# Optimization experiments

Measured on AMD Instinct MI355X. Metric: run time of the kernel, lower is better.

The kernel has to match this reference:

```python
import jax, jax.numpy as jnp
import numpy as np

D_MODEL = 1024
N_EXPERTS = 8
TOP_K = 2
D_FF = 4 * D_MODEL
BATCH, SEQ = 4, 2048


def setup_inputs() -> dict:
    key = jax.random.key(0)
    ks = jax.random.split(key, 7)
    s = 0.02
    return {
        "x": jax.random.normal(ks[0], (BATCH, SEQ, D_MODEL), dtype=jnp.float32),
        "Wg": jax.random.normal(ks[1], (D_MODEL, N_EXPERTS), dtype=jnp.float32) * s,
        "bg": jnp.zeros((N_EXPERTS,), dtype=jnp.float32),
        "W1": jax.random.normal(ks[2], (N_EXPERTS, D_MODEL, D_FF), dtype=jnp.float32) * s,
        "b1": jnp.zeros((N_EXPERTS, D_FF), dtype=jnp.float32),
        "W2": jax.random.normal(ks[3], (N_EXPERTS, D_FF, D_MODEL), dtype=jnp.float32) * s,
        "b2": jnp.zeros((N_EXPERTS, D_MODEL), dtype=jnp.float32),
    }


def reference(x, Wg, bg, W1, b1, W2, b2):
    B, S, D = x.shape
    T = B * S
    xf = x.reshape(T, D)  # [T, d_model]

    # Gating: top-k over softmax probabilities
    gate_logits = xf @ Wg + bg                      # [T, E]
    probs = jax.nn.softmax(gate_logits, axis=-1)
    weights, indices = jax.lax.top_k(probs, TOP_K)  # [T, K] each

    # Dense combine weights c[t, e] = sum_k weights[t,k] * (indices[t,k]==e)
    E = Wg.shape[1]
    c = jnp.zeros((T, E), dtype=x.dtype).at[jnp.arange(T)[:, None], indices].add(weights)

    # All-expert FFN as batched GEMMs (same math as masked per-expert loop)
    h = jnp.einsum('td,edf->etf', xf, W1) + b1[:, None, :]   # [E, T, d_ff]
    a = jax.nn.gelu(h, approximate=False)
    y = jnp.einsum('etf,efd->etd', a, W2) + b2[:, None, :]   # [E, T, d_model]

    out = jnp.einsum('te,etd->td', c, y).reshape(B, S, D)
    return out, gate_logits
```

## Files before the change

kernel.cpp:

```cpp
#include <hip/hip_runtime.h>
#include <hip/hip_bf16.h>
#include <math.h>

#define D_MODEL 1024
#define N_EXP   8
#define D_FF    4096
#define T_TOK   8192
#define NPAIR   (T_TOK * 2)
#define CAP_ROWS (NPAIR + N_EXP * 128)
#define MAX_TILES (CAP_ROWS / 128)

#define CHUNK_STRIDE 1056
#define TILE_BYTES   (8 * CHUNK_STRIDE)

typedef __attribute__((ext_vector_type(4)))  float  f32x4;
typedef __attribute__((ext_vector_type(16))) float  f32x16;
typedef __attribute__((ext_vector_type(8)))  __bf16 bf16x8;
typedef __attribute__((ext_vector_type(4)))  __bf16 bf16x4;

#define OFF_W1T   0
#define OFF_W2T   67108864
#define OFF_H     134217728
#define OFF_XR    276824064
#define OFF_META  312475648
#define M_PAIREXP 0
#define M_PAIRW   65536
#define M_ROW2P   131072
#define M_COUNTS  200704
#define M_PADST   200736
#define M_CURSOR  200768
#define M_T2E     201792
#define M_TROW    202336

__device__ __forceinline__ void async_copy16(const void* g, void* s) {
  __builtin_amdgcn_global_load_lds(
      (const __attribute__((address_space(1))) void*)g,
      (__attribute__((address_space(3))) void*)s, 16, 0, 0);
}

__device__ __forceinline__ float gelu_fast(float v) {
  float u = 1.5957691216057308f * (v + 0.044715f * v * v * v);
  return v * __builtin_amdgcn_rcpf(1.f + __expf(-u));
}

__global__ void k_gate(const float* __restrict__ x, const float* __restrict__ Wg,
                       const float* __restrict__ bg, float* __restrict__ logits_out,
                       int* __restrict__ pairExpert, float* __restrict__ pairW) {
  const int t    = blockIdx.x * 4 + (threadIdx.x >> 6);
  const int lane = threadIdx.x & 63;
  const float* xp = x + (size_t)t * D_MODEL;
  float acc[8];
#pragma unroll
  for (int e = 0; e < 8; e++) acc[e] = 0.f;
#pragma unroll
  for (int i = 0; i < 16; i++) {
    int d = i * 64 + lane;
    float xv = xp[d];
    const float4* wr = (const float4*)(Wg + d * 8);
    float4 w0 = wr[0], w1 = wr[1];
    acc[0] += xv * w0.x; acc[1] += xv * w0.y; acc[2] += xv * w0.z; acc[3] += xv * w0.w;
    acc[4] += xv * w1.x; acc[5] += xv * w1.y; acc[6] += xv * w1.z; acc[7] += xv * w1.w;
  }
#pragma unroll
  for (int e = 0; e < 8; e++)
#pragma unroll
    for (int off = 32; off > 0; off >>= 1) acc[e] += __shfl_down(acc[e], off);
  if (lane == 0) {
    float l[8];
#pragma unroll
    for (int e = 0; e < 8; e++) { l[e] = acc[e] + bg[e]; logits_out[t * 8 + e] = l[e]; }
    float m = l[0];
#pragma unroll
    for (int e = 1; e < 8; e++) m = fmaxf(m, l[e]);
    float p[8], s = 0.f;
#pragma unroll
    for (int e = 0; e < 8; e++) { p[e] = expf(l[e] - m); s += p[e]; }
    float inv = 1.0f / s;
    int i1 = 0;
#pragma unroll
    for (int e = 1; e < 8; e++) if (l[e] > l[i1]) i1 = e;
    int i2 = (i1 == 0) ? 1 : 0;
#pragma unroll
    for (int e = 0; e < 8; e++) if (e != i1 && l[e] > l[i2]) i2 = e;
    pairExpert[t * 2 + 0] = i1; pairW[t * 2 + 0] = p[i1] * inv;
    pairExpert[t * 2 + 1] = i2; pairW[t * 2 + 1] = p[i2] * inv;
  }
}

__global__ void k_init(int* __restrict__ row2pair) {
  int i = blockIdx.x * 256 + threadIdx.x;
  if (i < CAP_ROWS) row2pair[i] = -1;
}

__global__ void k_offsets(const int* __restrict__ pairExpert, int* __restrict__ counts,
                          int* __restrict__ padStart, int* __restrict__ cursor,
                          int* __restrict__ t2e, int* __restrict__ trow) {
  __shared__ int hist[8];
  int tid = threadIdx.x;
  if (tid < 8) hist[tid] = 0;
  __syncthreads();
  for (int i = tid; i < NPAIR; i += 256) atomicAdd(&hist[pairExpert[i]], 1);
  __syncthreads();
  if (tid == 0) {
    int run = 0, nt = 0;
    for (int e = 0; e < 8; e++) {
      counts[e] = hist[e]; padStart[e] = run; cursor[e * 32] = 0;
      int tiles = (hist[e] + 127) >> 7;
      for (int i = 0; i < tiles; i++) { t2e[nt] = e; trow[nt] = run + i * 128; nt++; }
      run += tiles * 128;
    }
    for (; nt < MAX_TILES; nt++) t2e[nt] = -1;
  }
}

__global__ void k_place(const int* __restrict__ pairExpert, const int* __restrict__ padStart,
                        int* __restrict__ cursor, int* __restrict__ row2pair) {
  int p = blockIdx.x * 256 + threadIdx.x;
  if (p >= NPAIR) return;
  int e = pairExpert[p];
  int r = atomicAdd(&cursor[e * 32], 1);
  row2pair[padStart[e] + r] = p;
}

__global__ void k_gather(const float* __restrict__ x, const int* __restrict__ row2pair,
                         __bf16* __restrict__ XR) {
  int row = blockIdx.x;
  int pair = row2pair[row];
  int c = threadIdx.x * 4;
  __bf16* dst = XR + (size_t)row * D_MODEL + c;
  if (pair < 0) {
    bf16x4 z = {(__bf16)0.f, (__bf16)0.f, (__bf16)0.f, (__bf16)0.f};
    *(bf16x4*)dst = z;
  } else {
    int t = pair >> 1;
    float4 v = *(const float4*)(x + (size_t)t * D_MODEL + c);
    bf16x4 o = {(__bf16)v.x, (__bf16)v.y, (__bf16)v.z, (__bf16)v.w};
    *(bf16x4*)dst = o;
  }
}

__global__ void k_convT(const float* __restrict__ in, __bf16* __restrict__ out,
                        int R, int C) {
  __shared__ __bf16 tile[64][68];
  int e = blockIdx.z;
  const float* ip = in + (size_t)e * R * C + (size_t)(blockIdx.y * 64) * C + blockIdx.x * 64;
  __bf16* op = out + (size_t)e * R * C + (size_t)(blockIdx.x * 64) * R + blockIdx.y * 64;
#pragma unroll
  for (int it = 0; it < 4; it++) {
    int idx = it * 1024 + threadIdx.x * 4;
    int lr = idx >> 6, lc = idx & 63;
    float4 v = *(const float4*)(ip + (size_t)lr * C + lc);
    bf16x4 o = {(__bf16)v.x, (__bf16)v.y, (__bf16)v.z, (__bf16)v.w};
    *(bf16x4*)&tile[lr][lc] = o;
  }
  __syncthreads();
#pragma unroll
  for (int it = 0; it < 4; it++) {
    int idx = it * 1024 + threadIdx.x * 4;
    int lc = idx >> 6, lr = idx & 63;
    bf16x4 o = {tile[lr + 0][lc], tile[lr + 1][lc], tile[lr + 2][lc], tile[lr + 3][lc]};
    *(bf16x4*)(op + (size_t)lc * R + lr) = o;
  }
}

__global__ __launch_bounds__(256) void k_gemm1(
    const __bf16* __restrict__ XR, const __bf16* __restrict__ W1T,
    const float* __restrict__ b1, __bf16* __restrict__ H,
    const int* __restrict__ t2e, const int* __restrict__ trow) {
  __shared__ __align__(16) char sA[TILE_BYTES];
  __shared__ __align__(16) char sB[TILE_BYTES];
  const int mt = blockIdx.y;
  const int e = t2e[mt];
  if (e < 0) return;
  const int rowBase = trow[mt];
  const int n0 = blockIdx.x * 128;
  const __bf16* Ab = XR + (size_t)rowBase * D_MODEL;
  const __bf16* Bb = W1T + (size_t)e * D_FF * D_MODEL + (size_t)n0 * D_MODEL;

  const int tid = threadIdx.x;
  const int rA = tid >> 2;
  const int kA = (tid & 3) * 8;
  const int lane = tid & 63;
  const int wave = tid >> 6;
  const int wm = (wave >> 1) * 64, wn = (wave & 1) * 64;
  const int l31 = lane & 31;
  const int half = lane >> 5;

  char* dA0 = sA + wave * CHUNK_STRIDE + lane * 16;
  char* dA1 = sA + (4 + wave) * CHUNK_STRIDE + lane * 16;
  char* dB0 = sB + wave * CHUNK_STRIDE + lane * 16;
  char* dB1 = sB + (4 + wave) * CHUNK_STRIDE + lane * 16;
  int mA0 = wm + l31, mA1 = wm + 32 + l31;
  const char* rA0 = sA + (mA0 >> 4) * CHUNK_STRIDE + (mA0 & 15) * 64 + half * 16;
  const char* rA1 = sA + (mA1 >> 4) * CHUNK_STRIDE + (mA1 & 15) * 64 + half * 16;
  int nB0 = wn + l31, nB1 = wn + 32 + l31;
  const char* rB0 = sB + (nB0 >> 4) * CHUNK_STRIDE + (nB0 & 15) * 64 + half * 16;
  const char* rB1 = sB + (nB1 >> 4) * CHUNK_STRIDE + (nB1 & 15) * 64 + half * 16;

  f32x16 acc[2][2];
#pragma unroll
  for (int i = 0; i < 2; i++)
#pragma unroll
    for (int j = 0; j < 2; j++) acc[i][j] = (f32x16)(0.f);

  for (int k0 = 0; k0 < D_MODEL; k0 += 32) {
    async_copy16(Ab + (size_t)rA * D_MODEL + k0 + kA,        dA0);
    async_copy16(Ab + (size_t)(rA + 64) * D_MODEL + k0 + kA, dA1);
    async_copy16(Bb + (size_t)rA * D_MODEL + k0 + kA,        dB0);
    async_copy16(Bb + (size_t)(rA + 64) * D_MODEL + k0 + kA, dB1);
    __syncthreads();
    bf16x8 af[2][2], bfr[2][2];
#pragma unroll
    for (int kc = 0; kc < 2; kc++) {
      af[0][kc]  = *(const bf16x8*)(rA0 + kc * 32);
      af[1][kc]  = *(const bf16x8*)(rA1 + kc * 32);
      bfr[0][kc] = *(const bf16x8*)(rB0 + kc * 32);
      bfr[1][kc] = *(const bf16x8*)(rB1 + kc * 32);
    }
#pragma unroll
    for (int kc = 0; kc < 2; kc++)
#pragma unroll
      for (int ti = 0; ti < 2; ti++)
#pragma unroll
        for (int tj = 0; tj < 2; tj++)
          acc[ti][tj] = __builtin_amdgcn_mfma_f32_32x32x16_bf16(af[ti][kc], bfr[tj][kc], acc[ti][tj], 0, 0, 0);
    __syncthreads();
  }
  int   colv[2]; float biasv[2];
#pragma unroll
  for (int tj = 0; tj < 2; tj++) {
    colv[tj] = n0 + wn + tj * 32 + l31;
    biasv[tj] = b1[e * D_FF + colv[tj]];
  }
#pragma unroll
  for (int ti = 0; ti < 2; ti++)
#pragma unroll
    for (int r = 0; r < 16; r++) {
      size_t row = (size_t)rowBase + wm + ti * 32 + (r & 3) + 8 * (r >> 2) + 4 * half;
#pragma unroll
      for (int tj = 0; tj < 2; tj++)
        H[row * D_FF + colv[tj]] = (__bf16)gelu_fast(acc[ti][tj][r] + biasv[tj]);
    }
}

__global__ __launch_bounds__(256) void k_gemm2(
    const __bf16* __restrict__ H, const __bf16* __restrict__ W2T,
    const float* __restrict__ b2, float* __restrict__ Ypair,
    const int* __restrict__ row2pair, const float* __restrict__ pairW,
    const int* __restrict__ t2e, const int* __restrict__ trow) {
  __shared__ __align__(16) char sA[TILE_BYTES];
  __shared__ __align__(16) char sB[TILE_BYTES];
  const int b = blockIdx.x;
  const int mt = (b >> 6) * 8 + (b & 7);
  const int nb = (b >> 3) & 7;
  const int e = t2e[mt];
  if (e < 0) return;
  const int rowBase = trow[mt];
  const int n0 = nb * 128;
  const __bf16* Ab = H + (size_t)rowBase * D_FF;
  const __bf16* Bb = W2T + (size_t)e * D_MODEL * D_FF + (size_t)n0 * D_FF;

  const int tid = threadIdx.x;
  const int rA = tid >> 2;
  const int kA = (tid & 3) * 8;
  const int lane = tid & 63;
  const int wave = tid >> 6;
  const int wm = (wave >> 1) * 64, wn = (wave & 1) * 64;
  const int l31 = lane & 31;
  const int half = lane >> 5;

  char* dA0 = sA + wave * CHUNK_STRIDE + lane * 16;
  char* dA1 = sA + (4 + wave) * CHUNK_STRIDE + lane * 16;
  char* dB0 = sB + wave * CHUNK_STRIDE + lane * 16;
  char* dB1 = sB + (4 + wave) * CHUNK_STRIDE + lane * 16;
  int mA0 = wm + l31, mA1 = wm + 32 + l31;
  const char* rA0 = sA + (mA0 >> 4) * CHUNK_STRIDE + (mA0 & 15) * 64 + half * 16;
  const char* rA1 = sA + (mA1 >> 4) * CHUNK_STRIDE + (mA1 & 15) * 64 + half * 16;
  int nB0 = wn + l31, nB1 = wn + 32 + l31;
  const char* rB0 = sB + (nB0 >> 4) * CHUNK_STRIDE + (nB0 & 15) * 64 + half * 16;
  const char* rB1 = sB + (nB1 >> 4) * CHUNK_STRIDE + (nB1 & 15) * 64 + half * 16;

  f32x16 acc[2][2];
#pragma unroll
  for (int i = 0; i < 2; i++)
#pragma unroll
    for (int j = 0; j < 2; j++) acc[i][j] = (f32x16)(0.f);

  for (int k0 = 0; k0 < D_FF; k0 += 32) {
    async_copy16(Ab + (size_t)rA * D_FF + k0 + kA,        dA0);
    async_copy16(Ab + (size_t)(rA + 64) * D_FF + k0 + kA, dA1);
    async_copy16(Bb + (size_t)rA * D_FF + k0 + kA,        dB0);
    async_copy16(Bb + (size_t)(rA + 64) * D_FF + k0 + kA, dB1);
    __syncthreads();
    bf16x8 af[2][2], bfr[2][2];
#pragma unroll
    for (int kc = 0; kc < 2; kc++) {
      af[0][kc]  = *(const bf16x8*)(rA0 + kc * 32);
      af[1][kc]  = *(const bf16x8*)(rA1 + kc * 32);
      bfr[0][kc] = *(const bf16x8*)(rB0 + kc * 32);
      bfr[1][kc] = *(const bf16x8*)(rB1 + kc * 32);
    }
#pragma unroll
    for (int kc = 0; kc < 2; kc++)
#pragma unroll
      for (int ti = 0; ti < 2; ti++)
#pragma unroll
        for (int tj = 0; tj < 2; tj++)
          acc[ti][tj] = __builtin_amdgcn_mfma_f32_32x32x16_bf16(af[ti][kc], bfr[tj][kc], acc[ti][tj], 0, 0, 0);
    __syncthreads();
  }
  int colv[2]; float biasv[2];
#pragma unroll
  for (int tj = 0; tj < 2; tj++) {
    colv[tj] = n0 + wn + tj * 32 + l31;
    biasv[tj] = b2[e * D_MODEL + colv[tj]];
  }
#pragma unroll
  for (int ti = 0; ti < 2; ti++)
#pragma unroll
    for (int r = 0; r < 16; r++) {
      int row = rowBase + wm + ti * 32 + (r & 3) + 8 * (r >> 2) + 4 * half;
      int pair = row2pair[row];
      if (pair < 0) continue;
      float w = pairW[pair];
#pragma unroll
      for (int tj = 0; tj < 2; tj++)
        Ypair[(size_t)pair * D_MODEL + colv[tj]] = w * (acc[ti][tj][r] + biasv[tj]);
    }
}

__global__ void k_combine(const float* __restrict__ Ypair, float* __restrict__ out) {
  size_t idx = (size_t)blockIdx.x * 256 + threadIdx.x;
  size_t t = idx >> 8, c4 = idx & 255;
  const float4* y4 = (const float4*)Ypair;
  float4 a = y4[(2 * t) * 256 + c4];
  float4 b = y4[(2 * t + 1) * 256 + c4];
  float4 o = {a.x + b.x, a.y + b.y, a.z + b.z, a.w + b.w};
  ((float4*)out)[idx] = o;
}

extern "C" void kernel_launch(void* const* d_in, const int* in_sizes, int n_in,
                              void* d_out, int out_size, void* d_ws, size_t ws_size,
                              hipStream_t stream) {
  const float* x  = (const float*)d_in[0];
  const float* Wg = (const float*)d_in[1];
  const float* bg = (const float*)d_in[2];
  const float* W1 = (const float*)d_in[3];
  const float* b1 = (const float*)d_in[4];
  const float* W2 = (const float*)d_in[5];
  const float* b2 = (const float*)d_in[6];
  float* out        = (float*)d_out;
  float* logits_out = out + (size_t)T_TOK * D_MODEL;

  char* ws = (char*)d_ws;
  __bf16* W1T = (__bf16*)(ws + OFF_W1T);
  __bf16* W2T = (__bf16*)(ws + OFF_W2T);
  __bf16* H   = (__bf16*)(ws + OFF_H);
  __bf16* XR  = (__bf16*)(ws + OFF_XR);
  float* Ypair = (float*)(ws + OFF_W1T);
  char* meta = ws + OFF_META;
  int*   pairExpert = (int*)(meta + M_PAIREXP);
  float* pairW      = (float*)(meta + M_PAIRW);
  int*   row2pair   = (int*)(meta + M_ROW2P);
  int*   counts     = (int*)(meta + M_COUNTS);
  int*   padStart   = (int*)(meta + M_PADST);
  int*   cursor     = (int*)(meta + M_CURSOR);
  int*   t2e        = (int*)(meta + M_T2E);
  int*   trow       = (int*)(meta + M_TROW);

  k_convT<<<dim3(D_FF / 64, D_MODEL / 64, N_EXP), 256, 0, stream>>>(W1, W1T, D_MODEL, D_FF);
  k_convT<<<dim3(D_MODEL / 64, D_FF / 64, N_EXP), 256, 0, stream>>>(W2, W2T, D_FF, D_MODEL);

  k_init<<<(CAP_ROWS + 255) / 256, 256, 0, stream>>>(row2pair);
  k_gate<<<T_TOK / 4, 256, 0, stream>>>(x, Wg, bg, logits_out, pairExpert, pairW);
  k_offsets<<<1, 256, 0, stream>>>(pairExpert, counts, padStart, cursor, t2e, trow);
  k_place<<<NPAIR / 256, 256, 0, stream>>>(pairExpert, padStart, cursor, row2pair);
  k_gather<<<CAP_ROWS, 256, 0, stream>>>(x, row2pair, XR);

  k_gemm1<<<dim3(D_FF / 128, MAX_TILES), 256, 0, stream>>>(XR, W1T, b1, H, t2e, trow);
  k_gemm2<<<MAX_TILES * (D_MODEL / 128), 256, 0, stream>>>(H, W2T, b2, Ypair, row2pair, pairW, t2e, trow);
  k_combine<<<(size_t)T_TOK * D_MODEL / 4 / 256, 256, 0, stream>>>(Ypair, out);
}
```

Before: 845.5 us.

## Rewrite expert GEMMs with larger tiles, double-buffered LDS and atomic combine

Both expert GEMMs move to 512-thread blocks with 256-row M tiles, a BK of 128, and XOR-swizzled LDS. Loads are double-buffered asynchronous copies interleaved between MFMA phases and gated by waitcnt and barriers, with raised wave priority around the MFMA sections. This is meant to improve data reuse and hide global-load latency. The second GEMM now atomically adds weighted results into a zeroed output, which removes the Ypair buffer and the combine kernel. The cost is atomic contention, a memset, and non-deterministic float summation order.

After: 952.5 us. 1.13x slower.

```diff
diff --git a/kernel.cpp b/kernel.cpp
--- a/kernel.cpp
+++ b/kernel.cpp
@@ -8,10 +8,8 @@
 #define T_TOK   8192
 #define NPAIR   (T_TOK * 2)
 #define CAP_ROWS (NPAIR + N_EXP * 128)
-#define MAX_TILES (CAP_ROWS / 128)
-
-#define CHUNK_STRIDE 1056
-#define TILE_BYTES   (8 * CHUNK_STRIDE)
+#define MAX_T256 72
+#define BKB 128
 
 typedef __attribute__((ext_vector_type(4)))  float  f32x4;
 typedef __attribute__((ext_vector_type(16))) float  f32x16;
@@ -31,11 +29,18 @@
 #define M_CURSOR  200768
 #define M_T2E     201792
 #define M_TROW    202336
+#define M_TLIM    202880
 
 __device__ __forceinline__ void async_copy16(const void* g, void* s) {
   __builtin_amdgcn_global_load_lds(
       (const __attribute__((address_space(1))) void*)g,
       (__attribute__((address_space(3))) void*)s, 16, 0, 0);
+}
+
+__device__ __forceinline__ void wg_barrier() {
+  asm volatile("" ::: "memory");
+  __builtin_amdgcn_s_barrier();
+  asm volatile("" ::: "memory");
 }
 
 __device__ __forceinline__ float gelu_fast(float v) {
@@ -94,7 +99,8 @@
 
 __global__ void k_offsets(const int* __restrict__ pairExpert, int* __restrict__ counts,
                           int* __restrict__ padStart, int* __restrict__ cursor,
-                          int* __restrict__ t2e, int* __restrict__ trow) {
+                          int* __restrict__ t2e, int* __restrict__ trow,
+                          int* __restrict__ tlim) {
   __shared__ int hist[8];
   int tid = threadIdx.x;
   if (tid < 8) hist[tid] = 0;
@@ -105,11 +111,16 @@
     int run = 0, nt = 0;
     for (int e = 0; e < 8; e++) {
       counts[e] = hist[e]; padStart[e] = run; cursor[e * 32] = 0;
-      int tiles = (hist[e] + 127) >> 7;
-      for (int i = 0; i < tiles; i++) { t2e[nt] = e; trow[nt] = run + i * 128; nt++; }
-      run += tiles * 128;
-    }
-    for (; nt < MAX_TILES; nt++) t2e[nt] = -1;
+      int rows = ((hist[e] + 127) >> 7) << 7;
+      for (int r0 = 0; r0 < rows; r0 += 256) {
+        t2e[nt] = e; trow[nt] = run + r0;
+        int rem = rows - r0;
+        tlim[nt] = rem < 256 ? rem : 256;
+        nt++;
+      }
+      run += rows;
+    }
+    for (; nt < MAX_T256; nt++) t2e[nt] = -1;
   }
 }
 
@@ -163,122 +174,204 @@
   }
 }
 
-__global__ __launch_bounds__(256) void k_gemm1(
+
+__global__ __launch_bounds__(512, 2) void k_gemm1(
     const __bf16* __restrict__ XR, const __bf16* __restrict__ W1T,
     const float* __restrict__ b1, __bf16* __restrict__ H,
-    const int* __restrict__ t2e, const int* __restrict__ trow) {
-  __shared__ __align__(16) char sA[TILE_BYTES];
-  __shared__ __align__(16) char sB[TILE_BYTES];
+    const int* __restrict__ t2e, const int* __restrict__ trow,
+    const int* __restrict__ tlim) {
+  __shared__ __align__(16) char lds[2][65536];
   const int mt = blockIdx.y;
   const int e = t2e[mt];
   if (e < 0) return;
   const int rowBase = trow[mt];
-  const int n0 = blockIdx.x * 128;
-  const __bf16* Ab = XR + (size_t)rowBase * D_MODEL;
-  const __bf16* Bb = W1T + (size_t)e * D_FF * D_MODEL + (size_t)n0 * D_MODEL;
+  const int lim = tlim[mt];
+  const int n0 = blockIdx.x * 256;
 
   const int tid = threadIdx.x;
-  const int rA = tid >> 2;
-  const int kA = (tid & 3) * 8;
-  const int lane = tid & 63;
-  const int wave = tid >> 6;
-  const int wm = (wave >> 1) * 64, wn = (wave & 1) * 64;
-  const int l31 = lane & 31;
-  const int half = lane >> 5;
-
-  char* dA0 = sA + wave * CHUNK_STRIDE + lane * 16;
-  char* dA1 = sA + (4 + wave) * CHUNK_STRIDE + lane * 16;
-  char* dB0 = sB + wave * CHUNK_STRIDE + lane * 16;
-  char* dB1 = sB + (4 + wave) * CHUNK_STRIDE + lane * 16;
-  int mA0 = wm + l31, mA1 = wm + 32 + l31;
-  const char* rA0 = sA + (mA0 >> 4) * CHUNK_STRIDE + (mA0 & 15) * 64 + half * 16;
-  const char* rA1 = sA + (mA1 >> 4) * CHUNK_STRIDE + (mA1 & 15) * 64 + half * 16;
-  int nB0 = wn + l31, nB1 = wn + 32 + l31;
-  const char* rB0 = sB + (nB0 >> 4) * CHUNK_STRIDE + (nB0 & 15) * 64 + half * 16;
-  const char* rB1 = sB + (nB1 >> 4) * CHUNK_STRIDE + (nB1 & 15) * 64 + half * 16;
-
-  f32x16 acc[2][2];
-#pragma unroll
-  for (int i = 0; i < 2; i++)
+  const int l = tid & 63;
+  const int w = tid >> 6;
+  const int wm = (w >> 2) * 128;
+  const int wn = (w & 3) * 64;
+  const int l31 = l & 31;
+  const int rsub = l >> 3;
+  const int sg = (l & 7) ^ rsub;
+
+  const char* srcA[4]; const char* srcB[4];
+#pragma unroll
+  for (int i = 0; i < 4; i++) {
+    int ra = rowBase + 8 * (w + 8 * i) + rsub;
+    if (ra > CAP_ROWS - 1) ra = CAP_ROWS - 1;
+    srcA[i] = (const char*)(XR + (size_t)ra * D_MODEL) + sg * 16;
+    int rb = n0 + 8 * (w + 8 * i) + rsub;
+    srcB[i] = (const char*)(W1T + (size_t)e * ((size_t)D_FF * D_MODEL)
+                                + (size_t)rb * D_MODEL) + sg * 16;
+  }
+  const int axr = ((l >> 5) ^ (l & 7)) << 4;
+
+  f32x16 acc[4][2];
+#pragma unroll
+  for (int i = 0; i < 4; i++)
 #pragma unroll
     for (int j = 0; j < 2; j++) acc[i][j] = (f32x16)(0.f);
 
-  for (int k0 = 0; k0 < D_MODEL; k0 += 32) {
-    async_copy16(Ab + (size_t)rA * D_MODEL + k0 + kA,        dA0);
-    async_copy16(Ab + (size_t)(rA + 64) * D_MODEL + k0 + kA, dA1);
-    async_copy16(Bb + (size_t)rA * D_MODEL + k0 + kA,        dB0);
-    async_copy16(Bb + (size_t)(rA + 64) * D_MODEL + k0 + kA, dB1);
-    __syncthreads();
-    bf16x8 af[2][2], bfr[2][2];
-#pragma unroll
-    for (int kc = 0; kc < 2; kc++) {
-      af[0][kc]  = *(const bf16x8*)(rA0 + kc * 32);
-      af[1][kc]  = *(const bf16x8*)(rA1 + kc * 32);
-      bfr[0][kc] = *(const bf16x8*)(rB0 + kc * 32);
-      bfr[1][kc] = *(const bf16x8*)(rB1 + kc * 32);
-    }
-#pragma unroll
-    for (int kc = 0; kc < 2; kc++)
-#pragma unroll
-      for (int ti = 0; ti < 2; ti++)
-#pragma unroll
-        for (int tj = 0; tj < 2; tj++)
-          acc[ti][tj] = __builtin_amdgcn_mfma_f32_32x32x16_bf16(af[ti][kc], bfr[tj][kc], acc[ti][tj], 0, 0, 0);
-    __syncthreads();
-  }
-  int   colv[2]; float biasv[2];
+  {
+    char* sAw = &lds[0][0];
+    char* sBw = sAw + 32768;
+#pragma unroll
+    for (int i = 0; i < 4; i++) {
+      async_copy16(srcA[i], sAw + (w + 8 * i) * 1024);
+      async_copy16(srcB[i], sBw + (w + 8 * i) * 1024);
+    }
+    asm volatile("s_waitcnt vmcnt(0)" ::: "memory");
+    wg_barrier();
+  }
+
+  bf16x8 A[2][4], B[2][4];
+#pragma unroll 2
+  for (int t = 0; t < 16; t++) {
+    const int slot = t & 1;
+    const char* sAr = &lds[0][0] + slot * 65536;
+    const char* sBr = sAr + 32768;
+    char* sAw = &lds[0][0] + (slot ^ 1) * 65536;
+    char* sBw = sAw + 32768;
+    const bool hn = (t + 1) < 16;
+    const size_t ko = (size_t)(t + 1) * BKB;
+
+    if (hn) {
+      async_copy16(srcA[0] + ko, sAw + w * 1024);
+      async_copy16(srcB[0] + ko, sBw + w * 1024);
+      asm volatile("s_waitcnt vmcnt(2)" ::: "memory");
+    } else {
+      asm volatile("s_waitcnt vmcnt(0)" ::: "memory");
+    }
+    wg_barrier();
+#pragma unroll
+    for (int f = 0; f < 2; f++)
+#pragma unroll
+      for (int kc = 0; kc < 4; kc++)
+        A[f][kc] = *(const bf16x8*)(sAr + (wm + f * 32 + l31) * BKB + (axr ^ (kc << 5)));
+#pragma unroll
+    for (int kc = 0; kc < 4; kc++)
+      B[0][kc] = *(const bf16x8*)(sBr + (wn + l31) * BKB + (axr ^ (kc << 5)));
+    __builtin_amdgcn_s_setprio(1);
+#pragma unroll
+    for (int kc = 0; kc < 4; kc++)
+#pragma unroll
+      for (int f = 0; f < 2; f++)
+        acc[f][0] = __builtin_amdgcn_mfma_f32_32x32x16_bf16(A[f][kc], B[0][kc], acc[f][0], 0, 0, 0);
+    __builtin_amdgcn_s_setprio(0);
+    wg_barrier();
+
+#pragma unroll
+    for (int kc = 0; kc < 4; kc++)
+      B[1][kc] = *(const bf16x8*)(sBr + (wn + 32 + l31) * BKB + (axr ^ (kc << 5)));
+    if (hn) {
+      async_copy16(srcA[1] + ko, sAw + (8 + w) * 1024);
+      async_copy16(srcB[1] + ko, sBw + (8 + w) * 1024);
+    }
+    wg_barrier();
+    __builtin_amdgcn_s_setprio(1);
+#pragma unroll
+    for (int kc = 0; kc < 4; kc++)
+#pragma unroll
+      for (int f = 0; f < 2; f++)
+        acc[f][1] = __builtin_amdgcn_mfma_f32_32x32x16_bf16(A[f][kc], B[1][kc], acc[f][1], 0, 0, 0);
+    __builtin_amdgcn_s_setprio(0);
+    wg_barrier();
+
+#pragma unroll
+    for (int f = 0; f < 2; f++)
+#pragma unroll
+      for (int kc = 0; kc < 4; kc++)
+        A[f][kc] = *(const bf16x8*)(sAr + (wm + 64 + f * 32 + l31) * BKB + (axr ^ (kc << 5)));
+    if (hn) {
+      async_copy16(srcA[2] + ko, sAw + (16 + w) * 1024);
+      async_copy16(srcB[2] + ko, sBw + (16 + w) * 1024);
+    }
+    wg_barrier();
+    __builtin_amdgcn_s_setprio(1);
+#pragma unroll
+    for (int kc = 0; kc < 4; kc++)
+#pragma unroll
+      for (int f = 0; f < 2; f++)
+        acc[2 + f][0] = __builtin_amdgcn_mfma_f32_32x32x16_bf16(A[f][kc], B[0][kc], acc[2 + f][0], 0, 0, 0);
+    __builtin_amdgcn_s_setprio(0);
+    wg_barrier();
+
+    if (hn) {
+      async_copy16(srcA[3] + ko, sAw + (24 + w) * 1024);
+      async_copy16(srcB[3] + ko, sBw + (24 + w) * 1024);
+    }
+    wg_barrier();
+    __builtin_amdgcn_s_setprio(1);
+#pragma unroll
+    for (int kc = 0; kc < 4; kc++)
+#pragma unroll
+      for (int f = 0; f < 2; f++)
+        acc[2 + f][1] = __builtin_amdgcn_mfma_f32_32x32x16_bf16(A[f][kc], B[1][kc], acc[2 + f][1], 0, 0, 0);
+    __builtin_amdgcn_s_setprio(0);
+    wg_barrier();
+  }
+
+  const int half = l >> 5;
+  int colv[2]; float biasv[2];
 #pragma unroll
   for (int tj = 0; tj < 2; tj++) {
     colv[tj] = n0 + wn + tj * 32 + l31;
     biasv[tj] = b1[e * D_FF + colv[tj]];
   }
 #pragma unroll
-  for (int ti = 0; ti < 2; ti++)
+  for (int ti = 0; ti < 4; ti++)
 #pragma unroll
     for (int r = 0; r < 16; r++) {
-      size_t row = (size_t)rowBase + wm + ti * 32 + (r & 3) + 8 * (r >> 2) + 4 * half;
-#pragma unroll
-      for (int tj = 0; tj < 2; tj++)
-        H[row * D_FF + colv[tj]] = (__bf16)gelu_fast(acc[ti][tj][r] + biasv[tj]);
-    }
-}
-
-__global__ __launch_bounds__(256) void k_gemm2(
+      int lr = wm + ti * 32 + (r & 3) + 8 * (r >> 2) + 4 * half;
+      if (lr < lim) {
+        size_t row = (size_t)(rowBase + lr);
+#pragma unroll
+        for (int tj = 0; tj < 2; tj++)
+          H[row * D_FF + colv[tj]] = (__bf16)gelu_fast(acc[ti][tj][r] + biasv[tj]);
+      }
+    }
+}
+
+__global__ __launch_bounds__(512, 2) void k_gemm2(
     const __bf16* __restrict__ H, const __bf16* __restrict__ W2T,
-    const float* __restrict__ b2, float* __restrict__ Ypair,
+    const float* __restrict__ b2, float* __restrict__ out,
     const int* __restrict__ row2pair, const float* __restrict__ pairW,
-    const int* __restrict__ t2e, const int* __restrict__ trow) {
-  __shared__ __align__(16) char sA[TILE_BYTES];
-  __shared__ __align__(16) char sB[TILE_BYTES];
-  const int b = blockIdx.x;
-  const int mt = (b >> 6) * 8 + (b & 7);
-  const int nb = (b >> 3) & 7;
+    const int* __restrict__ t2e, const int* __restrict__ trow,
+    const int* __restrict__ tlim) {
+  __shared__ __align__(16) char lds[2][49152];
+  const int mt = blockIdx.y;
   const int e = t2e[mt];
   if (e < 0) return;
   const int rowBase = trow[mt];
-  const int n0 = nb * 128;
-  const __bf16* Ab = H + (size_t)rowBase * D_FF;
-  const __bf16* Bb = W2T + (size_t)e * D_MODEL * D_FF + (size_t)n0 * D_FF;
+  const int lim = tlim[mt];
+  const int n0 = blockIdx.x * 128;
 
   const int tid = threadIdx.x;
-  const int rA = tid >> 2;
-  const int kA = (tid & 3) * 8;
-  const int lane = tid & 63;
-  const int wave = tid >> 6;
-  const int wm = (wave >> 1) * 64, wn = (wave & 1) * 64;
-  const int l31 = lane & 31;
-  const int half = lane >> 5;
-
-  char* dA0 = sA + wave * CHUNK_STRIDE + lane * 16;
-  char* dA1 = sA + (4 + wave) * CHUNK_STRIDE + lane * 16;
-  char* dB0 = sB + wave * CHUNK_STRIDE + lane * 16;
-  char* dB1 = sB + (4 + wave) * CHUNK_STRIDE + lane * 16;
-  int mA0 = wm + l31, mA1 = wm + 32 + l31;
-  const char* rA0 = sA + (mA0 >> 4) * CHUNK_STRIDE + (mA0 & 15) * 64 + half * 16;
-  const char* rA1 = sA + (mA1 >> 4) * CHUNK_STRIDE + (mA1 & 15) * 64 + half * 16;
-  int nB0 = wn + l31, nB1 = wn + 32 + l31;
-  const char* rB0 = sB + (nB0 >> 4) * CHUNK_STRIDE + (nB0 & 15) * 64 + half * 16;
-  const char* rB1 = sB + (nB1 >> 4) * CHUNK_STRIDE + (nB1 & 15) * 64 + half * 16;
+  const int l = tid & 63;
+  const int w = tid >> 6;
+  const int wm = (w >> 1) * 64;
+  const int wn = (w & 1) * 64;
+  const int l31 = l & 31;
+  const int rsub = l >> 3;
+  const int sg = (l & 7) ^ rsub;
+
+  const char* srcA[4]; const char* srcB[2];
+#pragma unroll
+  for (int i = 0; i < 4; i++) {
+    int ra = rowBase + 8 * (w + 8 * i) + rsub;
+    if (ra > CAP_ROWS - 1) ra = CAP_ROWS - 1;
+    srcA[i] = (const char*)(H + (size_t)ra * D_FF) + sg * 16;
+  }
+#pragma unroll
+  for (int i = 0; i < 2; i++) {
+    int rb = n0 + 8 * (w + 8 * i) + rsub;
+    srcB[i] = (const char*)(W2T + (size_t)e * ((size_t)D_MODEL * D_FF)
+                                + (size_t)rb * D_FF) + sg * 16;
+  }
+  const int axr = ((l >> 5) ^ (l & 7)) << 4;
 
   f32x16 acc[2][2];
 #pragma unroll
@@ -286,29 +379,74 @@
 #pragma unroll
     for (int j = 0; j < 2; j++) acc[i][j] = (f32x16)(0.f);
 
-  for (int k0 = 0; k0 < D_FF; k0 += 32) {
-    async_copy16(Ab + (size_t)rA * D_FF + k0 + kA,        dA0);
-    async_copy16(Ab + (size_t)(rA + 64) * D_FF + k0 + kA, dA1);
-    async_copy16(Bb + (size_t)rA * D_FF + k0 + kA,        dB0);
-    async_copy16(Bb + (size_t)(rA + 64) * D_FF + k0 + kA, dB1);
-    __syncthreads();
-    bf16x8 af[2][2], bfr[2][2];
-#pragma unroll
-    for (int kc = 0; kc < 2; kc++) {
-      af[0][kc]  = *(const bf16x8*)(rA0 + kc * 32);
-      af[1][kc]  = *(const bf16x8*)(rA1 + kc * 32);
-      bfr[0][kc] = *(const bf16x8*)(rB0 + kc * 32);
-      bfr[1][kc] = *(const bf16x8*)(rB1 + kc * 32);
-    }
-#pragma unroll
-    for (int kc = 0; kc < 2; kc++)
-#pragma unroll
-      for (int ti = 0; ti < 2; ti++)
-#pragma unroll
-        for (int tj = 0; tj < 2; tj++)
-          acc[ti][tj] = __builtin_amdgcn_mfma_f32_32x32x16_bf16(af[ti][kc], bfr[tj][kc], acc[ti][tj], 0, 0, 0);
-    __syncthreads();
-  }
+  {
+    char* sAw = &lds[0][0];
+    char* sBw = sAw + 32768;
+#pragma unroll
+    for (int i = 0; i < 4; i++) async_copy16(srcA[i], sAw + (w + 8 * i) * 1024);
+#pragma unroll
+    for (int i = 0; i < 2; i++) async_copy16(srcB[i], sBw + (w + 8 * i) * 1024);
+    asm volatile("s_waitcnt vmcnt(0)" ::: "memory");
+    wg_barrier();
+  }
+
+  bf16x8 A[4], B[2][4];
+#pragma unroll 2
+  for (int t = 0; t < 64; t++) {
+    const int slot = t & 1;
+    const char* sAr = &lds[0][0] + slot * 49152;
+    const char* sBr = sAr + 32768;
+    char* sAw = &lds[0][0] + (slot ^ 1) * 49152;
+    char* sBw = sAw + 32768;
+    const bool hn = (t + 1) < 64;
+    const size_t ko = (size_t)(t + 1) * BKB;
+
+    if (hn) {
+      async_copy16(srcA[0] + ko, sAw + w * 1024);
+      async_copy16(srcB[0] + ko, sBw + w * 1024);
+      async_copy16(srcA[1] + ko, sAw + (8 + w) * 1024);
+      async_copy16(srcB[1] + ko, sBw + (8 + w) * 1024);
+      asm volatile("s_waitcnt vmcnt(4)" ::: "memory");
+    } else {
+      asm volatile("s_waitcnt vmcnt(0)" ::: "memory");
+    }
+    wg_barrier();
+#pragma unroll
+    for (int kc = 0; kc < 4; kc++)
+      A[kc] = *(const bf16x8*)(sAr + (wm + l31) * BKB + (axr ^ (kc << 5)));
+#pragma unroll
+    for (int tj = 0; tj < 2; tj++)
+#pragma unroll
+      for (int kc = 0; kc < 4; kc++)
+        B[tj][kc] = *(const bf16x8*)(sBr + (wn + tj * 32 + l31) * BKB + (axr ^ (kc << 5)));
+    __builtin_amdgcn_s_setprio(1);
+#pragma unroll
+    for (int kc = 0; kc < 4; kc++)
+#pragma unroll
+      for (int tj = 0; tj < 2; tj++)
+        acc[0][tj] = __builtin_amdgcn_mfma_f32_32x32x16_bf16(A[kc], B[tj][kc], acc[0][tj], 0, 0, 0);
+    __builtin_amdgcn_s_setprio(0);
+    wg_barrier();
+
+#pragma unroll
+    for (int kc = 0; kc < 4; kc++)
+      A[kc] = *(const bf16x8*)(sAr + (wm + 32 + l31) * BKB + (axr ^ (kc << 5)));
+    if (hn) {
+      async_copy16(srcA[2] + ko, sAw + (16 + w) * 1024);
+      async_copy16(srcA[3] + ko, sAw + (24 + w) * 1024);
+    }
+    wg_barrier();
+    __builtin_amdgcn_s_setprio(1);
+#pragma unroll
+    for (int kc = 0; kc < 4; kc++)
+#pragma unroll
+      for (int tj = 0; tj < 2; tj++)
+        acc[1][tj] = __builtin_amdgcn_mfma_f32_32x32x16_bf16(A[kc], B[tj][kc], acc[1][tj], 0, 0, 0);
+    __builtin_amdgcn_s_setprio(0);
+    wg_barrier();
+  }
+
+  const int half = l >> 5;
   int colv[2]; float biasv[2];
 #pragma unroll
   for (int tj = 0; tj < 2; tj++) {
@@ -319,24 +457,16 @@
   for (int ti = 0; ti < 2; ti++)
 #pragma unroll
     for (int r = 0; r < 16; r++) {
-      int row = rowBase + wm + ti * 32 + (r & 3) + 8 * (r >> 2) + 4 * half;
-      int pair = row2pair[row];
+      int lr = wm + ti * 32 + (r & 3) + 8 * (r >> 2) + 4 * half;
+      if (lr >= lim) continue;
+      int pair = row2pair[rowBase + lr];
       if (pair < 0) continue;
-      float w = pairW[pair];
+      float pw = pairW[pair];
+      size_t tok = (size_t)(pair >> 1);
 #pragma unroll
       for (int tj = 0; tj < 2; tj++)
-        Ypair[(size_t)pair * D_MODEL + colv[tj]] = w * (acc[ti][tj][r] + biasv[tj]);
-    }
-}
-
-__global__ void k_combine(const float* __restrict__ Ypair, float* __restrict__ out) {
-  size_t idx = (size_t)blockIdx.x * 256 + threadIdx.x;
-  size_t t = idx >> 8, c4 = idx & 255;
-  const float4* y4 = (const float4*)Ypair;
-  float4 a = y4[(2 * t) * 256 + c4];
-  float4 b = y4[(2 * t + 1) * 256 + c4];
-  float4 o = {a.x + b.x, a.y + b.y, a.z + b.z, a.w + b.w};
-  ((float4*)out)[idx] = o;
+        atomicAdd(out + tok * D_MODEL + colv[tj], pw * (acc[ti][tj][r] + biasv[tj]));
+    }
 }
 
 extern "C" void kernel_launch(void* const* d_in, const int* in_sizes, int n_in,
@@ -357,7 +487,6 @@
   __bf16* W2T = (__bf16*)(ws + OFF_W2T);
   __bf16* H   = (__bf16*)(ws + OFF_H);
   __bf16* XR  = (__bf16*)(ws + OFF_XR);
-  float* Ypair = (float*)(ws + OFF_W1T);
   char* meta = ws + OFF_META;
   int*   pairExpert = (int*)(meta + M_PAIREXP);
   float* pairW      = (float*)(meta + M_PAIRW);
@@ -367,17 +496,20 @@
   int*   cursor     = (int*)(meta + M_CURSOR);
   int*   t2e        = (int*)(meta + M_T2E);
   int*   trow       = (int*)(meta + M_TROW);
+  int*   tlim       = (int*)(meta + M_TLIM);
+
+  hipMemsetAsync(out, 0, (size_t)T_TOK * D_MODEL * sizeof(float), stream);
 
   k_convT<<<dim3(D_FF / 64, D_MODEL / 64, N_EXP), 256, 0, stream>>>(W1, W1T, D_MODEL, D_FF);
   k_convT<<<dim3(D_MODEL / 64, D_FF / 64, N_EXP), 256, 0, stream>>>(W2, W2T, D_FF, D_MODEL);
 
   k_init<<<(CAP_ROWS + 255) / 256, 256, 0, stream>>>(row2pair);
   k_gate<<<T_TOK / 4, 256, 0, stream>>>(x, Wg, bg, logits_out, pairExpert, pairW);
-  k_offsets<<<1, 256, 0, stream>>>(pairExpert, counts, padStart, cursor, t2e, trow);
+  k_offsets<<<1, 256, 0, stream>>>(pairExpert, counts, padStart, cursor, t2e, trow, tlim);
   k_place<<<NPAIR / 256, 256, 0, stream>>>(pairExpert, padStart, cursor, row2pair);
   k_gather<<<CAP_ROWS, 256, 0, stream>>>(x, row2pair, XR);
 
-  k_gemm1<<<dim3(D_FF / 128, MAX_TILES), 256, 0, stream>>>(XR, W1T, b1, H, t2e, trow);
-  k_gemm2<<<MAX_TILES * (D_MODEL / 128), 256, 0, stream>>>(H, W2T, b2, Ypair, row2pair, pairW, t2e, trow);
-  k_combine<<<(size_t)T_TOK * D_MODEL / 4 / 256, 256, 0, stream>>>(Ypair, out);
-}
+  k_gemm1<<<dim3(D_FF / 256, MAX_T256), 512, 0, stream>>>(XR, W1T, b1, H, t2e, trow, tlim);
+  k_gemm2<<<dim3(D_MODEL / 128, MAX_T256), 512, 0, stream>>>(H, W2T, b2, out, row2pair, pairW,
+                                                             t2e, trow, tlim);
+}
```

## Triple-buffer GEMM mainloops with XOR-swizzled LDS and atomic combine

Applied to the files above, without the earlier changes.

Both expert GEMMs move from a single-buffered LDS tile with two barriers per k-step to a three-stage ring of async copies, waiting on vmcnt so loads for later k-steps overlap MFMA work. LDS uses an XOR swizzle instead of padded chunk strides, MFMA runs at raised wave priority, and gemm1 gets grouped tile ordering for L2 reuse. The separate combine kernel and Ypair buffer go away: gemm2 atomically adds weighted results into a zeroed output. Atomics make float summation order nondeterministic, add a memset, and 48KB of LDS per block may limit occupancy.

New measurement: 859.7 us. About the same (+1.7%).

```diff
diff --git a/kernel.cpp b/kernel.cpp
--- a/kernel.cpp
+++ b/kernel.cpp
@@ -9,9 +9,6 @@
 #define NPAIR   (T_TOK * 2)
 #define CAP_ROWS (NPAIR + N_EXP * 128)
 #define MAX_TILES (CAP_ROWS / 128)
-
-#define CHUNK_STRIDE 1056
-#define TILE_BYTES   (8 * CHUNK_STRIDE)
 
 typedef __attribute__((ext_vector_type(4)))  float  f32x4;
 typedef __attribute__((ext_vector_type(16))) float  f32x16;
@@ -163,122 +160,152 @@
   }
 }
 
-__global__ __launch_bounds__(256) void k_gemm1(
+
+#define STG(SW, T)                                                         \
+  do {                                                                     \
+    size_t _ko = (size_t)(T) * 64;                                         \
+    async_copy16(srcA0 + _ko, (SW) + w * 1024);                            \
+    async_copy16(srcA1 + _ko, (SW) + (w + 4) * 1024);                      \
+    async_copy16(srcB0 + _ko, (SW) + 8192 + w * 1024);                     \
+    async_copy16(srcB1 + _ko, (SW) + 8192 + (w + 4) * 1024);               \
+  } while (0)
+
+#define LDF(SR)                                                            \
+  do {                                                                     \
+    _Pragma("unroll")                                                      \
+    for (int mi = 0; mi < 2; mi++)                                         \
+      _Pragma("unroll")                                                    \
+      for (int kc = 0; kc < 2; kc++)                                       \
+        Af[mi][kc] = *(const bf16x8*)((SR) + (wm + mi * 32 + l31) * 64 + (aoff ^ (kc << 5))); \
+    _Pragma("unroll")                                                      \
+    for (int nj = 0; nj < 2; nj++)                                         \
+      _Pragma("unroll")                                                    \
+      for (int kc = 0; kc < 2; kc++)                                       \
+        Bf[nj][kc] = *(const bf16x8*)((SR) + 8192 + (wn + nj * 32 + l31) * 64 + (aoff ^ (kc << 5))); \
+  } while (0)
+
+#define MFM                                                                \
+  do {                                                                     \
+    __builtin_amdgcn_s_setprio(1);                                         \
+    _Pragma("unroll")                                                      \
+    for (int kc = 0; kc < 2; kc++)                                         \
+      _Pragma("unroll")                                                    \
+      for (int mi = 0; mi < 2; mi++)                                       \
+        _Pragma("unroll")                                                  \
+        for (int nj = 0; nj < 2; nj++)                                     \
+          acc[mi][nj] = __builtin_amdgcn_mfma_f32_32x32x16_bf16(           \
+              Af[mi][kc], Bf[nj][kc], acc[mi][nj], 0, 0, 0);               \
+    __builtin_amdgcn_s_setprio(0);                                         \
+  } while (0)
+
+#define ENDW(N)                                                            \
+  do {                                                                     \
+    __builtin_amdgcn_sched_barrier(0);                                     \
+    asm volatile("s_waitcnt vmcnt(" #N ")" ::: "memory");                  \
+    __builtin_amdgcn_s_barrier();                                          \
+    asm volatile("" ::: "memory");                                         \
+  } while (0)
+
+#define BODY(SR, SW, T) \
+  do { bf16x8 Af[2][2], Bf[2][2]; STG(SW, T); LDF(SR); MFM; ENDW(4); } while (0)
+#define BODY_N0(SR) \
+  do { bf16x8 Af[2][2], Bf[2][2]; LDF(SR); MFM; ENDW(0); } while (0)
+#define BODY_LAST(SR) \
+  do { bf16x8 Af[2][2], Bf[2][2]; LDF(SR); MFM; } while (0)
+
+__global__ __launch_bounds__(256, 3) void k_gemm1(
     const __bf16* __restrict__ XR, const __bf16* __restrict__ W1T,
     const float* __restrict__ b1, __bf16* __restrict__ H,
     const int* __restrict__ t2e, const int* __restrict__ trow) {
-  __shared__ __align__(16) char sA[TILE_BYTES];
-  __shared__ __align__(16) char sB[TILE_BYTES];
-  const int mt = blockIdx.y;
-  const int e = t2e[mt];
-  if (e < 0) return;
-  const int rowBase = trow[mt];
-  const int n0 = blockIdx.x * 128;
-  const __bf16* Ab = XR + (size_t)rowBase * D_MODEL;
-  const __bf16* Bb = W1T + (size_t)e * D_FF * D_MODEL + (size_t)n0 * D_MODEL;
-
-  const int tid = threadIdx.x;
-  const int rA = tid >> 2;
-  const int kA = (tid & 3) * 8;
-  const int lane = tid & 63;
-  const int wave = tid >> 6;
-  const int wm = (wave >> 1) * 64, wn = (wave & 1) * 64;
-  const int l31 = lane & 31;
-  const int half = lane >> 5;
-
-  char* dA0 = sA + wave * CHUNK_STRIDE + lane * 16;
-  char* dA1 = sA + (4 + wave) * CHUNK_STRIDE + lane * 16;
-  char* dB0 = sB + wave * CHUNK_STRIDE + lane * 16;
-  char* dB1 = sB + (4 + wave) * CHUNK_STRIDE + lane * 16;
-  int mA0 = wm + l31, mA1 = wm + 32 + l31;
-  const char* rA0 = sA + (mA0 >> 4) * CHUNK_STRIDE + (mA0 & 15) * 64 + half * 16;
-  const char* rA1 = sA + (mA1 >> 4) * CHUNK_STRIDE + (mA1 & 15) * 64 + half * 16;
-  int nB0 = wn + l31, nB1 = wn + 32 + l31;
-  const char* rB0 = sB + (nB0 >> 4) * CHUNK_STRIDE + (nB0 & 15) * 64 + half * 16;
-  const char* rB1 = sB + (nB1 >> 4) * CHUNK_STRIDE + (nB1 & 15) * 64 + half * 16;
-
-  f32x16 acc[2][2];
-#pragma unroll
-  for (int i = 0; i < 2; i++)
-#pragma unroll
-    for (int j = 0; j < 2; j++) acc[i][j] = (f32x16)(0.f);
-
-  for (int k0 = 0; k0 < D_MODEL; k0 += 32) {
-    async_copy16(Ab + (size_t)rA * D_MODEL + k0 + kA,        dA0);
-    async_copy16(Ab + (size_t)(rA + 64) * D_MODEL + k0 + kA, dA1);
-    async_copy16(Bb + (size_t)rA * D_MODEL + k0 + kA,        dB0);
-    async_copy16(Bb + (size_t)(rA + 64) * D_MODEL + k0 + kA, dB1);
-    __syncthreads();
-    bf16x8 af[2][2], bfr[2][2];
-#pragma unroll
-    for (int kc = 0; kc < 2; kc++) {
-      af[0][kc]  = *(const bf16x8*)(rA0 + kc * 32);
-      af[1][kc]  = *(const bf16x8*)(rA1 + kc * 32);
-      bfr[0][kc] = *(const bf16x8*)(rB0 + kc * 32);
-      bfr[1][kc] = *(const bf16x8*)(rB1 + kc * 32);
-    }
-#pragma unroll
-    for (int kc = 0; kc < 2; kc++)
-#pragma unroll
-      for (int ti = 0; ti < 2; ti++)
-#pragma unroll
-        for (int tj = 0; tj < 2; tj++)
-          acc[ti][tj] = __builtin_amdgcn_mfma_f32_32x32x16_bf16(af[ti][kc], bfr[tj][kc], acc[ti][tj], 0, 0, 0);
-    __syncthreads();
-  }
-  int   colv[2]; float biasv[2];
-#pragma unroll
-  for (int tj = 0; tj < 2; tj++) {
-    colv[tj] = n0 + wn + tj * 32 + l31;
-    biasv[tj] = b1[e * D_FF + colv[tj]];
-  }
-#pragma unroll
-  for (int ti = 0; ti < 2; ti++)
-#pragma unroll
-    for (int r = 0; r < 16; r++) {
-      size_t row = (size_t)rowBase + wm + ti * 32 + (r & 3) + 8 * (r >> 2) + 4 * half;
-#pragma unroll
-      for (int tj = 0; tj < 2; tj++)
-        H[row * D_FF + colv[tj]] = (__bf16)gelu_fast(acc[ti][tj][r] + biasv[tj]);
-    }
-}
-
-__global__ __launch_bounds__(256) void k_gemm2(
-    const __bf16* __restrict__ H, const __bf16* __restrict__ W2T,
-    const float* __restrict__ b2, float* __restrict__ Ypair,
-    const int* __restrict__ row2pair, const float* __restrict__ pairW,
-    const int* __restrict__ t2e, const int* __restrict__ trow) {
-  __shared__ __align__(16) char sA[TILE_BYTES];
-  __shared__ __align__(16) char sB[TILE_BYTES];
-  const int b = blockIdx.x;
-  const int mt = (b >> 6) * 8 + (b & 7);
-  const int nb = (b >> 3) & 7;
+  __shared__ __align__(16) char lds[3][16384];
+  const int bid = blockIdx.x;
+  const int q = bid >> 8, w8 = bid & 255;
+  const int nb = w8 >> 3, mt = q * 8 + (w8 & 7);
   const int e = t2e[mt];
   if (e < 0) return;
   const int rowBase = trow[mt];
   const int n0 = nb * 128;
-  const __bf16* Ab = H + (size_t)rowBase * D_FF;
+
+  const int tid = threadIdx.x;
+  const int l = tid & 63, w = tid >> 6;
+  const int wm = (w >> 1) * 64, wn = (w & 1) * 64;
+  const int l31 = l & 31, half = l >> 5;
+  const int rsub = l >> 2;
+  const int sg = (l & 3) ^ ((l >> 3) & 3);
+  const int aoff = ((half ^ ((l >> 1) & 3)) << 4);
+
+  const char* srcA0 = (const char*)(XR + (size_t)(rowBase + 16 * w + rsub) * D_MODEL) + sg * 16;
+  const char* srcA1 = srcA0 + (size_t)64 * D_MODEL * 2;
+  const __bf16* Bb = W1T + (size_t)e * D_FF * D_MODEL + (size_t)n0 * D_MODEL;
+  const char* srcB0 = (const char*)(Bb + (size_t)(16 * w + rsub) * D_MODEL) + sg * 16;
+  const char* srcB1 = srcB0 + (size_t)64 * D_MODEL * 2;
+
+  f32x16 acc[2][2];
+#pragma unroll
+  for (int i = 0; i < 2; i++)
+#pragma unroll
+    for (int j = 0; j < 2; j++) acc[i][j] = (f32x16)(0.f);
+
+  char* s0 = &lds[0][0]; char* s1 = &lds[1][0]; char* s2 = &lds[2][0];
+
+  STG(s0, 0);
+  STG(s1, 1);
+  ENDW(4);
+
+#pragma unroll 1
+  for (int g = 0; g < 10; g++) {
+    int t = 3 * g;
+    BODY(s0, s2, t + 2);
+    BODY(s1, s0, t + 3);
+    BODY(s2, s1, t + 4);
+  }
+  BODY_N0(s0);
+  BODY_LAST(s1);
+
+  int colv[2]; float biasv[2];
+#pragma unroll
+  for (int nj = 0; nj < 2; nj++) {
+    colv[nj] = n0 + wn + nj * 32 + l31;
+    biasv[nj] = b1[e * D_FF + colv[nj]];
+  }
+#pragma unroll
+  for (int mi = 0; mi < 2; mi++)
+#pragma unroll
+    for (int r = 0; r < 16; r++) {
+      size_t row = (size_t)rowBase + wm + mi * 32 + (r & 3) + 8 * (r >> 2) + 4 * half;
+#pragma unroll
+      for (int nj = 0; nj < 2; nj++)
+        H[row * D_FF + colv[nj]] = (__bf16)gelu_fast(acc[mi][nj][r] + biasv[nj]);
+    }
+}
+
+__global__ __launch_bounds__(256, 3) void k_gemm2(
+    const __bf16* __restrict__ H, const __bf16* __restrict__ W2T,
+    const float* __restrict__ b2, float* __restrict__ out,
+    const int* __restrict__ row2pair, const float* __restrict__ pairW,
+    const int* __restrict__ t2e, const int* __restrict__ trow) {
+  __shared__ __align__(16) char lds[3][16384];
+  const int bid = blockIdx.x;
+  const int q = bid >> 6, w8 = bid & 63;
+  const int nb = w8 >> 3, mt = q * 8 + (w8 & 7);
+  const int e = t2e[mt];
+  if (e < 0) return;
+  const int rowBase = trow[mt];
+  const int n0 = nb * 128;
+
+  const int tid = threadIdx.x;
+  const int l = tid & 63, w = tid >> 6;
+  const int wm = (w >> 1) * 64, wn = (w & 1) * 64;
+  const int l31 = l & 31, half = l >> 5;
+  const int rsub = l >> 2;
+  const int sg = (l & 3) ^ ((l >> 3) & 3);
+  const int aoff = ((half ^ ((l >> 1) & 3)) << 4);
+
+  const char* srcA0 = (const char*)(H + (size_t)(rowBase + 16 * w + rsub) * D_FF) + sg * 16;
+  const char* srcA1 = srcA0 + (size_t)64 * D_FF * 2;
   const __bf16* Bb = W2T + (size_t)e * D_MODEL * D_FF + (size_t)n0 * D_FF;
-
-  const int tid = threadIdx.x;
-  const int rA = tid >> 2;
-  const int kA = (tid & 3) * 8;
-  const int lane = tid & 63;
-  const int wave = tid >> 6;
-  const int wm = (wave >> 1) * 64, wn = (wave & 1) * 64;
-  const int l31 = lane & 31;
-  const int half = lane >> 5;
-
-  char* dA0 = sA + wave * CHUNK_STRIDE + lane * 16;
-  char* dA1 = sA + (4 + wave) * CHUNK_STRIDE + lane * 16;
-  char* dB0 = sB + wave * CHUNK_STRIDE + lane * 16;
-  char* dB1 = sB + (4 + wave) * CHUNK_STRIDE + lane * 16;
-  int mA0 = wm + l31, mA1 = wm + 32 + l31;
-  const char* rA0 = sA + (mA0 >> 4) * CHUNK_STRIDE + (mA0 & 15) * 64 + half * 16;
-  const char* rA1 = sA + (mA1 >> 4) * CHUNK_STRIDE + (mA1 & 15) * 64 + half * 16;
-  int nB0 = wn + l31, nB1 = wn + 32 + l31;
-  const char* rB0 = sB + (nB0 >> 4) * CHUNK_STRIDE + (nB0 & 15) * 64 + half * 16;
-  const char* rB1 = sB + (nB1 >> 4) * CHUNK_STRIDE + (nB1 & 15) * 64 + half * 16;
+  const char* srcB0 = (const char*)(Bb + (size_t)(16 * w + rsub) * D_FF) + sg * 16;
+  const char* srcB1 = srcB0 + (size_t)64 * D_FF * 2;
 
   f32x16 acc[2][2];
 #pragma unroll
@@ -286,57 +313,41 @@
 #pragma unroll
     for (int j = 0; j < 2; j++) acc[i][j] = (f32x16)(0.f);
 
-  for (int k0 = 0; k0 < D_FF; k0 += 32) {
-    async_copy16(Ab + (size_t)rA * D_FF + k0 + kA,        dA0);
-    async_copy16(Ab + (size_t)(rA + 64) * D_FF + k0 + kA, dA1);
-    async_copy16(Bb + (size_t)rA * D_FF + k0 + kA,        dB0);
-    async_copy16(Bb + (size_t)(rA + 64) * D_FF + k0 + kA, dB1);
-    __syncthreads();
-    bf16x8 af[2][2], bfr[2][2];
-#pragma unroll
-    for (int kc = 0; kc < 2; kc++) {
-      af[0][kc]  = *(const bf16x8*)(rA0 + kc * 32);
-      af[1][kc]  = *(const bf16x8*)(rA1 + kc * 32);
-      bfr[0][kc] = *(const bf16x8*)(rB0 + kc * 32);
-      bfr[1][kc] = *(const bf16x8*)(rB1 + kc * 32);
-    }
-#pragma unroll
-    for (int kc = 0; kc < 2; kc++)
-#pragma unroll
-      for (int ti = 0; ti < 2; ti++)
-#pragma unroll
-        for (int tj = 0; tj < 2; tj++)
-          acc[ti][tj] = __builtin_amdgcn_mfma_f32_32x32x16_bf16(af[ti][kc], bfr[tj][kc], acc[ti][tj], 0, 0, 0);
-    __syncthreads();
-  }
+  char* s0 = &lds[0][0]; char* s1 = &lds[1][0]; char* s2 = &lds[2][0];
+
+  STG(s0, 0);
+  STG(s1, 1);
+  ENDW(4);
+
+#pragma unroll 1
+  for (int g = 0; g < 42; g++) {
+    int t = 3 * g;
+    BODY(s0, s2, t + 2);
+    BODY(s1, s0, t + 3);
+    BODY(s2, s1, t + 4);
+  }
+  BODY_N0(s0);
+  BODY_LAST(s1);
+
   int colv[2]; float biasv[2];
 #pragma unroll
-  for (int tj = 0; tj < 2; tj++) {
-    colv[tj] = n0 + wn + tj * 32 + l31;
-    biasv[tj] = b2[e * D_MODEL + colv[tj]];
-  }
-#pragma unroll
-  for (int ti = 0; ti < 2; ti++)
+  for (int nj = 0; nj < 2; nj++) {
+    colv[nj] = n0 + wn + nj * 32 + l31;
+    biasv[nj] = b2[e * D_MODEL + colv[nj]];
+  }
+#pragma unroll
+  for (int mi = 0; mi < 2; mi++)
 #pragma unroll
     for (int r = 0; r < 16; r++) {
-      int row = rowBase + wm + ti * 32 + (r & 3) + 8 * (r >> 2) + 4 * half;
+      int row = rowBase + wm + mi * 32 + (r & 3) + 8 * (r >> 2) + 4 * half;
       int pair = row2pair[row];
       if (pair < 0) continue;
-      float w = pairW[pair];
-#pragma unroll
-      for (int tj = 0; tj < 2; tj++)
-        Ypair[(size_t)pair * D_MODEL + colv[tj]] = w * (acc[ti][tj][r] + biasv[tj]);
+      float pw = pairW[pair];
+      size_t tok = (size_t)(pair >> 1);
+#pragma unroll
+      for (int nj = 0; nj < 2; nj++)
+        atomicAdd(out + tok * D_MODEL + colv[nj], pw * (acc[mi][nj][r] + biasv[nj]));
     }
-}
-
-__global__ void k_combine(const float* __restrict__ Ypair, float* __restrict__ out) {
-  size_t idx = (size_t)blockIdx.x * 256 + threadIdx.x;
-  size_t t = idx >> 8, c4 = idx & 255;
-  const float4* y4 = (const float4*)Ypair;
-  float4 a = y4[(2 * t) * 256 + c4];
-  float4 b = y4[(2 * t + 1) * 256 + c4];
-  float4 o = {a.x + b.x, a.y + b.y, a.z + b.z, a.w + b.w};
-  ((float4*)out)[idx] = o;
 }
 
 extern "C" void kernel_launch(void* const* d_in, const int* in_sizes, int n_in,
@@ -357,7 +368,6 @@
   __bf16* W2T = (__bf16*)(ws + OFF_W2T);
   __bf16* H   = (__bf16*)(ws + OFF_H);
   __bf16* XR  = (__bf16*)(ws + OFF_XR);
-  float* Ypair = (float*)(ws + OFF_W1T);
   char* meta = ws + OFF_META;
   int*   pairExpert = (int*)(meta + M_PAIREXP);
   float* pairW      = (float*)(meta + M_PAIRW);
@@ -368,6 +378,8 @@
   int*   t2e        = (int*)(meta + M_T2E);
   int*   trow       = (int*)(meta + M_TROW);
 
+  hipMemsetAsync(out, 0, (size_t)T_TOK * D_MODEL * sizeof(float), stream);
+
   k_convT<<<dim3(D_FF / 64, D_MODEL / 64, N_EXP), 256, 0, stream>>>(W1, W1T, D_MODEL, D_FF);
   k_convT<<<dim3(D_MODEL / 64, D_FF / 64, N_EXP), 256, 0, stream>>>(W2, W2T, D_FF, D_MODEL);
 
@@ -377,7 +389,6 @@
   k_place<<<NPAIR / 256, 256, 0, stream>>>(pairExpert, padStart, cursor, row2pair);
   k_gather<<<CAP_ROWS, 256, 0, stream>>>(x, row2pair, XR);
 
-  k_gemm1<<<dim3(D_FF / 128, MAX_TILES), 256, 0, stream>>>(XR, W1T, b1, H, t2e, trow);
-  k_gemm2<<<MAX_TILES * (D_MODEL / 128), 256, 0, stream>>>(H, W2T, b2, Ypair, row2pair, pairW, t2e, trow);
-  k_combine<<<(size_t)T_TOK * D_MODEL / 4 / 256, 256, 0, stream>>>(Ypair, out);
-}
+  k_gemm1<<<(MAX_TILES / 8) * 256, 256, 0, stream>>>(XR, W1T, b1, H, t2e, trow);
+  k_gemm2<<<(MAX_TILES / 8) * 64, 256, 0, stream>>>(H, W2T, b2, out, row2pair, pairW, t2e, trow);
+}
```
